# Performance work log

Hardware: AMD Instinct MI355X
Metric: run time of the kernel (lower is better)

The kernel has to match this reference:

```python
import jax, jax.numpy as jnp
import numpy as np
from jax import lax

EPS = 1e-5

def _conv(x, w, b, pad):
    y = lax.conv_general_dilated(x, w, (1, 1), [(pad, pad), (pad, pad)],
                                 dimension_numbers=('NCHW', 'OIHW', 'NCHW'))
    return y + b[None, :, None, None]

def _bn(x, g, b, m, v):
    # eval-mode BatchNorm2d with running stats
    scale = g * lax.rsqrt(v + EPS)
    return x * scale[None, :, None, None] + (b - m * scale)[None, :, None, None]

def setup_inputs() -> dict:
    key = jax.random.key(0)
    ks = jax.random.split(key, 16)
    B, C, H, W = 16, 64, 128, 128
    C2 = 2 * C
    d = {}
    d['x'] = jax.random.normal(ks[0], (B, C, H, W), jnp.float32)
    # fc1: Conv2d(C,C,3,p=1) + BN(C)
    d['fc1_w'] = jax.random.normal(ks[1], (C, C, 3, 3), jnp.float32) * 0.05
    d['fc1_b'] = jax.random.normal(ks[2], (C,), jnp.float32) * 0.05
    d['bn1_g'] = jnp.ones((C,), jnp.float32)
    d['bn1_b'] = jnp.zeros((C,), jnp.float32)
    d['bn1_m'] = jax.random.normal(ks[3], (C,), jnp.float32) * 0.05
    d['bn1_v'] = jax.random.uniform(ks[4], (C,), jnp.float32) * 0.5 + 0.5
    # graph_conv.nn: Conv2d(2C,2C,1) + BN(2C) + GELU
    d['gc_w'] = jax.random.normal(ks[5], (C2, C2, 1, 1), jnp.float32) * 0.05
    d['gc_b'] = jax.random.normal(ks[6], (C2,), jnp.float32) * 0.05
    d['bng_g'] = jnp.ones((C2,), jnp.float32)
    d['bng_b'] = jnp.zeros((C2,), jnp.float32)
    d['bng_m'] = jax.random.normal(ks[7], (C2,), jnp.float32) * 0.05
    d['bng_v'] = jax.random.uniform(ks[8], (C2,), jnp.float32) * 0.5 + 0.5
    # fc2: Conv2d(2C,C,3,p=1) + BN(C)
    d['fc2_w'] = jax.random.normal(ks[9], (C, C2, 3, 3), jnp.float32) * 0.05
    d['fc2_b'] = jax.random.normal(ks[10], (C,), jnp.float32) * 0.05
    d['bn2_g'] = jnp.ones((C,), jnp.float32)
    d['bn2_b'] = jnp.zeros((C,), jnp.float32)
    d['bn2_m'] = jax.random.normal(ks[11], (C,), jnp.float32) * 0.05
    d['bn2_v'] = jax.random.uniform(ks[12], (C,), jnp.float32) * 0.5 + 0.5
    return d

def reference(x, fc1_w, fc1_b, bn1_g, bn1_b, bn1_m, bn1_v,
              gc_w, gc_b, bng_g, bng_b, bng_m, bng_v,
              fc2_w, fc2_b, bn2_g, bn2_b, bn2_m, bn2_v):
    # fc1
    h = _bn(_conv(x, fc1_w, fc1_b, 1), bn1_g, bn1_b, bn1_m, bn1_v)
    # MRConv4dSP: strided self-attention over superpatch tokens
    sel = h[:, :, ::4, ::4]                          # [B,C,h4,w4]
    B, C, h4, w4 = sel.shape
    q = sel.reshape(B, C, h4 * w4).transpose(0, 2, 1)  # [B,N,C]
    scale = C ** (-0.5)
    att = jax.nn.softmax(jnp.einsum('bnc,bmc->bnm', q, q) * scale, axis=-1)
    o = jnp.einsum('bnm,bmc->bnc', att, q)           # [B,N,C]
    o = o.transpose(0, 2, 1).reshape(B, C, h4, w4)
    o = jnp.repeat(jnp.repeat(o, 4, axis=2), 4, axis=3)
    g = jnp.concatenate([h, o], axis=1)              # [B,2C,H,W]
    g = jax.nn.gelu(_bn(_conv(g, gc_w, gc_b, 0), bng_g, bng_b, bng_m, bng_v),
                    approximate=False)
    # fc2 + residual (drop_path=0 -> identity)
    y = _bn(_conv(g, fc2_w, fc2_b, 1), bn2_g, bn2_b, bn2_m, bn2_v)
    return y + x
```

## Files before the change

### kernel.cpp

```cpp
#include <hip/hip_runtime.h>
#include <math.h>

#define EPSV 1e-5f

typedef __bf16 bf16;
using bf16x8 = __attribute__((ext_vector_type(8))) __bf16;
using bf16x4 = __attribute__((ext_vector_type(4))) __bf16;
using bf16x2 = __attribute__((ext_vector_type(2))) __bf16;
using f32x4  = __attribute__((ext_vector_type(4))) float;

static __device__ __forceinline__ f32x4 mfma16(bf16x8 a, bf16x8 b, f32x4 c) {
    return __builtin_amdgcn_mfma_f32_16x16x32_bf16(a, b, c, 0, 0, 0);
}
static __device__ __forceinline__ f32x4 zero4() {
    f32x4 z = {0.f, 0.f, 0.f, 0.f};
    return z;
}

typedef __attribute__((address_space(1))) const char g_char_t;
typedef __attribute__((address_space(3))) char lds_char_t;
static __device__ __forceinline__ void gll16(const void* g, void* l) {
    __builtin_amdgcn_global_load_lds((g_char_t*)g, (lds_char_t*)l, 16, 0, 0);
}

static __device__ __forceinline__ float gelu_f(float v) {
    float z = fabsf(v) * 0.70710678118f;
    float t = __builtin_amdgcn_rcpf(1.f + 0.3275911f * z);
    float poly = t * (0.254829592f + t * (-0.284496736f + t * (1.421413741f +
                 t * (-1.453152027f + t * 1.061405429f))));
    float e = __expf(-z * z);
    float erfv = copysignf(1.f - poly * e, v);
    return 0.5f * v * (1.f + erfv);
}

static __device__ __forceinline__ void prep3x3_one(const float* w, bf16* wt,
                                                   int t, int CIN)
{
    int cout = t / CIN, ci = t - cout * CIN;
    int cci = ci >> 5, lg = (ci >> 3) & 3, j = ci & 7;
    int mi = cout >> 4, lix = cout & 15;
#pragma unroll
    for (int kgt = 0; kgt < 9; ++kgt) {
        float v = w[(size_t)t * 9 + kgt];
        wt[((((size_t)kgt * (CIN >> 5) + cci) * 4 + mi) * 64 + lg * 16 + lix) * 8 + j]
            = (bf16)v;
    }
}

__global__ __launch_bounds__(256) void prep_all(
    const float* __restrict__ fc1_w, const float* __restrict__ fc2_w,
    const float* __restrict__ gc_w,
    bf16* __restrict__ wt1, bf16* __restrict__ wt2, bf16* __restrict__ wtg,
    float* __restrict__ zb)
{
    int bx = blockIdx.x, tid = threadIdx.x;
    if (bx < 16) {
        prep3x3_one(fc1_w, wt1, bx * 256 + tid, 64);
    } else if (bx < 48) {
        prep3x3_one(fc2_w, wt2, (bx - 16) * 256 + tid, 128);
    } else {
        if (bx == 48 && tid < 64)
            ((float4*)zb)[tid] = make_float4(0.f, 0.f, 0.f, 0.f);
        int t = (bx - 48) * 256 + tid;
        int cout = t >> 7, ci = t & 127;
        int ks = ci >> 5, lg = (ci >> 3) & 3, j = ci & 7;
        wtg[(((size_t)(ks * 4 + lg) * 128) + cout) * 8 + j] = (bf16)gc_w[t];
    }
}

__global__ __launch_bounds__(256) void cvt_x_nhwc(const float* __restrict__ x,
                                                  bf16* __restrict__ xb)
{
    __shared__ float t_lds[64 * 68];
    const int bx = blockIdx.x;
    const int b  = blockIdx.y;
    const int y  = bx >> 1, x0 = (bx & 1) * 64;
    const int tid = threadIdx.x;

    for (int f = tid; f < 64 * 16; f += 256) {
        int c = f >> 4, xu = f & 15;
        float4 v = *(const float4*)&x[((size_t)(b * 64 + c) << 14) + (y << 7) + x0 + xu * 4];
        t_lds[(xu * 4 + 0) * 68 + c] = v.x;
        t_lds[(xu * 4 + 1) * 68 + c] = v.y;
        t_lds[(xu * 4 + 2) * 68 + c] = v.z;
        t_lds[(xu * 4 + 3) * 68 + c] = v.w;
    }
    __syncthreads();
    for (int f = tid; f < 64 * 8; f += 256) {
        int xx = f >> 3, cu = f & 7;
        const float* p = &t_lds[xx * 68 + cu * 8];
        bf16x8 v;
#pragma unroll
        for (int j = 0; j < 8; ++j) v[j] = (bf16)p[j];
        *(bf16x8*)&xb[((size_t)((b * 128 + y) * 128) + x0 + xx) * 64 + cu * 8] = v;
    }
}

template<int CIN, int OUTMODE>
__global__ __launch_bounds__(512) void conv3x3_mfma(
    const bf16* __restrict__ in, const bf16* __restrict__ wt,
    const float* __restrict__ bias,
    const float* __restrict__ bg, const float* __restrict__ bb,
    const float* __restrict__ bm, const float* __restrict__ bv,
    const bf16* __restrict__ resid, const bf16* __restrict__ zb,
    void* __restrict__ outp, bf16* __restrict__ qout)
{
    constexpr int NC = CIN >> 5;
    __shared__ bf16 in_lds[2][672 * 32];
    __shared__ bf16 w_lds[2][36 * 512];

    const int wg = blockIdx.x;
    const int v  = (wg & 7) * 64 + (wg >> 3);
    const int tile = v & 31, b = v >> 5;
    const int x0 = (tile & 1) * 64;
    const int y0 = (tile >> 1) * 8;
    const int tid  = threadIdx.x;
    const int wid  = tid >> 6;
    const int lane = tid & 63;
    const int lix  = lane & 15, lg = lane >> 4;

    int goff[6]; bool gok[6];
#pragma unroll
    for (int i = 0; i < 6; ++i) {
        int chunk = wid + 8 * i;
        int f = chunk * 64 + lane;
        int pix = f >> 2, u = f & 3;
        int sw = (pix & 3) ^ ((pix >> 2) & 3);
        int ug = u ^ sw;
        int iy = pix / 66, ix = pix - iy * 66;
        int gy = y0 + iy - 1, gx = x0 + ix - 1;
        gok[i]  = (chunk < 42) && (pix < 660) &&
                  (unsigned)gy < 128u && (unsigned)gx < 128u;
        goff[i] = ((b * 128 + gy) * 128 + gx) * CIN + ug * 8;
    }
    int rd[9];
#pragma unroll
    for (int kg = 0; kg < 3; ++kg)
#pragma unroll
        for (int t = 0; t < 3; ++t) {
            int pix0 = (wid + kg) * 66 + lix + t;
            int sw = (pix0 & 3) ^ ((pix0 >> 2) & 3);
            rd[kg * 3 + t] = pix0 * 32 + ((lg ^ sw) << 3);
        }

    f32x4 acc[4][4];
#pragma unroll
    for (int i = 0; i < 4; ++i)
#pragma unroll
        for (int j = 0; j < 4; ++j) acc[i][j] = zero4();

    auto issue_in = [&](int cci, int buf) {
#pragma unroll
        for (int i = 0; i < 6; ++i) {
            int chunk = wid + 8 * i;
            if (chunk < 42) {
                const void* src = gok[i] ? (const void*)(in + goff[i] + cci * 32)
                                         : (const void*)zb;
                gll16(src, (char*)&in_lds[buf][0] + chunk * 1024);
            }
        }
    };
    auto issue_w = [&](int cci, int buf) {
#pragma unroll
        for (int i = 0; i < 5; ++i) {
            int chunk = wid + 8 * i;
            if (chunk < 36) {
                const bf16* src = wt + ((size_t)(chunk >> 2) * NC + cci) * 2048
                                     + (chunk & 3) * 512 + lane * 8;
                gll16(src, (char*)&w_lds[buf][0] + chunk * 1024);
            }
        }
    };
    auto compute = [&](int buf) {
        bf16x8 afA[4], bfA[4], afB[4], bfB[4];
#pragma unroll
        for (int mi = 0; mi < 4; ++mi)
            afA[mi] = *(const bf16x8*)&w_lds[buf][(0 * 4 + mi) * 512 + lane * 8];
#pragma unroll
        for (int nj = 0; nj < 4; ++nj)
            bfA[nj] = *(const bf16x8*)&in_lds[buf][rd[0] + nj * 512];
#pragma unroll
        for (int kgt = 0; kgt < 9; ++kgt) {
            bf16x8* afC = (kgt & 1) ? afB : afA;
            bf16x8* bfC = (kgt & 1) ? bfB : bfA;
            bf16x8* afN = (kgt & 1) ? afA : afB;
            bf16x8* bfN = (kgt & 1) ? bfA : bfB;
            if (kgt < 8) {
#pragma unroll
                for (int mi = 0; mi < 4; ++mi)
                    afN[mi] = *(const bf16x8*)&w_lds[buf][((kgt + 1) * 4 + mi) * 512 + lane * 8];
#pragma unroll
                for (int nj = 0; nj < 4; ++nj)
                    bfN[nj] = *(const bf16x8*)&in_lds[buf][rd[kgt + 1] + nj * 512];
            }
            __builtin_amdgcn_sched_barrier(0);
#pragma unroll
            for (int nj = 0; nj < 4; ++nj)
#pragma unroll
                for (int mi = 0; mi < 4; ++mi)
                    acc[mi][nj] = mfma16(afC[mi], bfC[nj], acc[mi][nj]);
            __builtin_amdgcn_sched_barrier(0);
        }
    };

    issue_in(0, 0);
    issue_w(0, 0);
#pragma unroll 1
    for (int c = 0; c < NC; ++c) {
        if (c + 1 < NC) {
            issue_in(c + 1, (c + 1) & 1);
            issue_w(c + 1, (c + 1) & 1);
            if (wid < 2)      asm volatile("s_waitcnt vmcnt(11)" ::: "memory");
            else if (wid < 4) asm volatile("s_waitcnt vmcnt(10)" ::: "memory");
            else              asm volatile("s_waitcnt vmcnt(9)"  ::: "memory");
        } else {
            asm volatile("s_waitcnt vmcnt(0)" ::: "memory");
        }
        __builtin_amdgcn_s_barrier();
        __builtin_amdgcn_sched_barrier(0);
        compute(c & 1);
        __builtin_amdgcn_s_barrier();
    }

    if (OUTMODE == 0) {
        bf16* out = (bf16*)outp;
        bf16* stg = &in_lds[0][0];
#pragma unroll
        for (int mi = 0; mi < 4; ++mi) {
            float A[4], Bc[4];
#pragma unroll
            for (int r = 0; r < 4; ++r) {
                int c = mi * 16 + lg * 4 + r;
                float s = bg[c] * rsqrtf(bv[c] + EPSV);
                A[r]  = s;
                Bc[r] = bias[c] * s + bb[c] - bm[c] * s;
            }
#pragma unroll
            for (int nj = 0; nj < 4; ++nj) {
                int px = nj * 16 + lix;
                bf16x4 vv;
#pragma unroll
                for (int r = 0; r < 4; ++r)
                    vv[r] = (bf16)(acc[mi][nj][r] * A[r] + Bc[r]);
                *(bf16x4*)&stg[(wid * 64 + px) * 68 + mi * 16 + lg * 4] = vv;
            }
        }
        __syncthreads();
#pragma unroll
        for (int k = 0; k < 8; ++k) {
            int idx = k * 512 + tid;
            int row = idx >> 9, rem = idx & 511;
            int px = rem >> 3, cu = rem & 7;
            bf16x8 vv = *(const bf16x8*)&stg[(row * 64 + px) * 68 + cu * 8];
            *(bf16x8*)&out[((size_t)((b * 128 + y0 + row) * 128)
                            + x0 + px) * 64 + cu * 8] = vv;
        }
        if (qout && tid < 256) {
            int row4 = (tid >> 7) * 4;
            int rem  = tid & 127;
            int px4  = (rem >> 3) * 4, cu = rem & 7;
            int gy = y0 + row4, gx = x0 + px4;
            int n = ((gy >> 2) << 5) + (gx >> 2);
            bf16x8 vv = *(const bf16x8*)&stg[(row4 * 64 + px4) * 68 + cu * 8];
            *(bf16x8*)&qout[((size_t)(b * 1024 + n)) * 64 + cu * 8] = vv;
        }
    } else {
        float* out = (float*)outp;
        const int gy = y0 + wid;
#pragma unroll
        for (int mi = 0; mi < 4; ++mi) {
            float A[4], Bc[4];
#pragma unroll
            for (int r = 0; r < 4; ++r) {
                int c = mi * 16 + lg * 4 + r;
                float s = bg[c] * rsqrtf(bv[c] + EPSV);
                A[r]  = s;
                Bc[r] = bias[c] * s + bb[c] - bm[c] * s;
            }
#pragma unroll
            for (int nj = 0; nj < 4; ++nj) {
                int px = x0 + nj * 16 + lix;
                bf16x4 rv = *(const bf16x4*)&resid[((size_t)((b * 128 + gy) * 128) + px) * 64
                                                   + mi * 16 + lg * 4];
#pragma unroll
                for (int r = 0; r < 4; ++r) {
                    int c = mi * 16 + lg * 4 + r;
                    size_t oi = ((size_t)(b * 64 + c) << 14) + (gy << 7) + px;
                    out[oi] = acc[mi][nj][r] * A[r] + Bc[r] + (float)rv[r];
                }
            }
        }
    }
}

__global__ __launch_bounds__(256) void attn_fused(const bf16* __restrict__ q,
                                                  bf16* __restrict__ o)
{
    __shared__ bf16 qn[64 * 72];
    __shared__ bf16 kn[128 * 72];
    __shared__ bf16 vt[64 * 136];
    __shared__ bf16 pl[4][16 * 136];
    __shared__ __align__(16) float fac[4][16];
    const int n0 = blockIdx.x * 64, b = blockIdx.y;
    const int tid = threadIdx.x, w = tid >> 6, lane = tid & 63;
    const int lix = lane & 15, lg = lane >> 4;
    const bf16* qb = q + ((size_t)b << 16);

    for (int f = tid; f < 512; f += 256) {
        int row = f >> 3, cu = f & 7;
        *(bf16x8*)&qn[row * 72 + cu * 8] =
            *(const bf16x8*)&qb[(size_t)(n0 + row) * 64 + cu * 8];
    }

    float m_run = -3.0e38f, l_run = 0.f;
    f32x4 oacc[4];
#pragma unroll
    for (int ct = 0; ct < 4; ++ct) oacc[ct] = zero4();

    for (int mt = 0; mt < 1024; mt += 128) {
        __syncthreads();
        for (int f = tid; f < 1024; f += 256) {
            int row = f >> 3, cu = f & 7;
            *(bf16x8*)&kn[row * 72 + cu * 8] =
                *(const bf16x8*)&qb[(size_t)(mt + row) * 64 + cu * 8];
        }
        for (int f = tid; f < 512; f += 256) {
            int mp = f >> 3, cu = f & 7;
            int m = mp * 2;
            bf16x8 a = *(const bf16x8*)&qb[(size_t)(mt + m) * 64 + cu * 8];
            bf16x8 c = *(const bf16x8*)&qb[(size_t)(mt + m + 1) * 64 + cu * 8];
#pragma unroll
            for (int j = 0; j < 8; ++j) {
                bf16x2 pr = {a[j], c[j]};
                *(bf16x2*)&vt[(cu * 8 + j) * 136 + m] = pr;
            }
        }
        __syncthreads();

        bf16x8 bq0 = *(const bf16x8*)&qn[(w * 16 + lix) * 72 + lg * 8];
        bf16x8 bq1 = *(const bf16x8*)&qn[(w * 16 + lix) * 72 + 32 + lg * 8];

        f32x4 s[8];
#pragma unroll
        for (int t = 0; t < 8; ++t) {
            bf16x8 a0 = *(const bf16x8*)&kn[(t * 16 + lix) * 72 + lg * 8];
            bf16x8 a1 = *(const bf16x8*)&kn[(t * 16 + lix) * 72 + 32 + lg * 8];
            s[t] = mfma16(a0, bq0, zero4());
            s[t] = mfma16(a1, bq1, s[t]);
        }

        float mx = -3.0e38f;
#pragma unroll
        for (int t = 0; t < 8; ++t)
#pragma unroll
            for (int r = 0; r < 4; ++r) { s[t][r] *= 0.125f; mx = fmaxf(mx, s[t][r]); }
        mx = fmaxf(mx, __shfl_xor(mx, 16));
        mx = fmaxf(mx, __shfl_xor(mx, 32));
        float m_new = fmaxf(m_run, mx);
        float alpha = __expf(m_run - m_new);

        float psum = 0.f;
#pragma unroll
        for (int t = 0; t < 8; ++t) {
            float p0 = __expf(s[t][0] - m_new), p1 = __expf(s[t][1] - m_new);
            float p2 = __expf(s[t][2] - m_new), p3 = __expf(s[t][3] - m_new);
            psum += (p0 + p1) + (p2 + p3);
            bf16x2 v01 = {(bf16)p0, (bf16)p1};
            bf16x2 v23 = {(bf16)p2, (bf16)p3};
            *(bf16x2*)&pl[w][lix * 136 + t * 16 + lg * 4]     = v01;
            *(bf16x2*)&pl[w][lix * 136 + t * 16 + lg * 4 + 2] = v23;
        }
        psum += __shfl_xor(psum, 16);
        psum += __shfl_xor(psum, 32);
        l_run = l_run * alpha + psum;
        m_run = m_new;
        if (lg == 0) fac[w][lix] = alpha;

        float4 a4 = *(const float4*)&fac[w][lg * 4];
        float aa[4] = {a4.x, a4.y, a4.z, a4.w};
#pragma unroll
        for (int ct = 0; ct < 4; ++ct)
#pragma unroll
            for (int r = 0; r < 4; ++r) oacc[ct][r] *= aa[r];

#pragma unroll
        for (int kk = 0; kk < 4; ++kk) {
            bf16x8 pa = *(const bf16x8*)&pl[w][lix * 136 + kk * 32 + lg * 8];
#pragma unroll
            for (int ct = 0; ct < 4; ++ct) {
                bf16x8 bv = *(const bf16x8*)&vt[(ct * 16 + lix) * 136 + kk * 32 + lg * 8];
                oacc[ct] = mfma16(pa, bv, oacc[ct]);
            }
        }
    }

    if (lg == 0) fac[w][lix] = l_run;
    float4 l4 = *(const float4*)&fac[w][lg * 4];
    float ll[4] = {1.f / l4.x, 1.f / l4.y, 1.f / l4.z, 1.f / l4.w};
#pragma unroll
    for (int ct = 0; ct < 4; ++ct)
#pragma unroll
        for (int r = 0; r < 4; ++r) {
            int n = n0 + w * 16 + lg * 4 + r;
            int c = ct * 16 + lix;
            o[((size_t)(b * 1024 + n)) * 64 + c] = (bf16)(oacc[ct][r] * ll[r]);
        }
}

__global__ __launch_bounds__(256) void conv1x1_mfma(
    const bf16* __restrict__ h, const bf16* __restrict__ ov,
    const bf16* __restrict__ wt, const float* __restrict__ bias,
    const float* __restrict__ bg, const float* __restrict__ bb,
    const float* __restrict__ bm, const float* __restrict__ bv,
    bf16* __restrict__ g)
{
    __shared__ bf16 in1[128 * 136];
    const int y = blockIdx.x, b = blockIdx.y;
    const int tid = threadIdx.x;
    const int wid = tid >> 6, lane = tid & 63;
    const int lix = lane & 15, lg = lane >> 4;
    const int wm = wid >> 1, wn = wid & 1;

    for (int f = tid; f < 128 * 16; f += 256) {
        int px = f >> 4, cu = f & 15;
        bf16x8 v;
        if (cu < 8) {
            v = *(const bf16x8*)&h[((size_t)((b * 128 + y) * 128 + px)) * 64 + cu * 8];
        } else {
            int n = ((y >> 2) << 5) + (px >> 2);
            v = *(const bf16x8*)&ov[((size_t)(b * 1024 + n)) * 64 + (cu - 8) * 8];
        }
        *(bf16x8*)&in1[px * 136 + cu * 8] = v;
    }
    __syncthreads();

    f32x4 acc[4][4];
#pragma unroll
    for (int i = 0; i < 4; ++i)
#pragma unroll
        for (int j = 0; j < 4; ++j) acc[i][j] = zero4();

#pragma unroll
    for (int ks = 0; ks < 4; ++ks) {
        bf16x8 af[4], bfv[4];
#pragma unroll
        for (int mi = 0; mi < 4; ++mi)
            af[mi] = *(const bf16x8*)&wt[(((size_t)(ks * 4 + lg) * 128) + wm * 64 + mi * 16 + lix) * 8];
#pragma unroll
        for (int nj = 0; nj < 4; ++nj)
            bfv[nj] = *(const bf16x8*)&in1[(wn * 64 + nj * 16 + lix) * 136 + ks * 32 + lg * 8];
#pragma unroll
        for (int mi = 0; mi < 4; ++mi)
#pragma unroll
            for (int nj = 0; nj < 4; ++nj)
                acc[mi][nj] = mfma16(af[mi], bfv[nj], acc[mi][nj]);
    }

    __syncthreads();
    bf16* stg = in1;
#pragma unroll
    for (int mi = 0; mi < 4; ++mi) {
        float A[4], Bc[4];
#pragma unroll
        for (int r = 0; r < 4; ++r) {
            int c = wm * 64 + mi * 16 + lg * 4 + r;
            float s = bg[c] * rsqrtf(bv[c] + EPSV);
            A[r]  = s;
            Bc[r] = bias[c] * s + bb[c] - bm[c] * s;
        }
#pragma unroll
        for (int nj = 0; nj < 4; ++nj) {
            int px = wn * 64 + nj * 16 + lix;
            bf16x4 vv;
#pragma unroll
            for (int r = 0; r < 4; ++r)
                vv[r] = (bf16)gelu_f(acc[mi][nj][r] * A[r] + Bc[r]);
            *(bf16x4*)&stg[px * 132 + wm * 64 + mi * 16 + lg * 4] = vv;
        }
    }
    __syncthreads();
#pragma unroll
    for (int k = 0; k < 8; ++k) {
        int idx = k * 256 + tid;
        int px = idx >> 4, cu = idx & 15;
        bf16x8 v = *(const bf16x8*)&stg[px * 132 + cu * 8];
        *(bf16x8*)&g[((size_t)((b * 128 + y) * 128) + px) * 128 + cu * 8] = v;
    }
}

extern "C" void kernel_launch(void* const* d_in, const int* in_sizes, int n_in,
                              void* d_out, int out_size, void* d_ws, size_t ws_size,
                              hipStream_t stream)
{
    const float* x     = (const float*)d_in[0];
    const float* fc1_w = (const float*)d_in[1];
    const float* fc1_b = (const float*)d_in[2];
    const float* bn1_g = (const float*)d_in[3];
    const float* bn1_b = (const float*)d_in[4];
    const float* bn1_m = (const float*)d_in[5];
    const float* bn1_v = (const float*)d_in[6];
    const float* gc_w  = (const float*)d_in[7];
    const float* gc_b  = (const float*)d_in[8];
    const float* bng_g = (const float*)d_in[9];
    const float* bng_b = (const float*)d_in[10];
    const float* bng_m = (const float*)d_in[11];
    const float* bng_v = (const float*)d_in[12];
    const float* fc2_w = (const float*)d_in[13];
    const float* fc2_b = (const float*)d_in[14];
    const float* bn2_g = (const float*)d_in[15];
    const float* bn2_b = (const float*)d_in[16];
    const float* bn2_m = (const float*)d_in[17];
    const float* bn2_v = (const float*)d_in[18];

    char* wsb = (char*)d_ws;
    bf16* x_bf = (bf16*)wsb;
    bf16* h    = (bf16*)(wsb + 33554432);
    bf16* g    = (bf16*)(wsb + 67108864);
    bf16* q    = (bf16*)(wsb + 134217728);
    bf16* o    = (bf16*)(wsb + 136314880);
    bf16* wt1  = (bf16*)(wsb + 138412032);
    bf16* wt2  = (bf16*)(wsb + 138485760);
    bf16* wtg  = (bf16*)(wsb + 138633216);
    bf16* zb   = (bf16*)(wsb + 138665984);

    prep_all<<<112, 256, 0, stream>>>(fc1_w, fc2_w, gc_w, wt1, wt2, wtg,
                                      (float*)zb);

    cvt_x_nhwc<<<dim3(256, 16), 256, 0, stream>>>(x, x_bf);

    conv3x3_mfma<64, 0><<<512, 512, 0, stream>>>(
        x_bf, wt1, fc1_b, bn1_g, bn1_b, bn1_m, bn1_v, nullptr, zb, h, q);

    attn_fused<<<dim3(16, 16), 256, 0, stream>>>(q, o);

    conv1x1_mfma<<<dim3(128, 16), 256, 0, stream>>>(
        h, o, wtg, gc_b, bng_g, bng_b, bng_m, bng_v, g);

    conv3x3_mfma<128, 1><<<512, 512, 0, stream>>>(
        g, wt2, fc2_b, bn2_g, bn2_b, bn2_m, bn2_v, x_bf, zb, (float*)d_out, nullptr);
}
```

Before: 179.4 us.

## Fuse 1x1 conv+BN+GELU into attention kernel and merge prep with input conversion

The attention kernel now keeps its output tile in LDS and computes the 1x1 graph conv, BN and GELU for the 8 rows of pixels that correspond to its 64 tokens. It streams h through a double-buffered global_load_lds pipeline with swizzled layout. This removes the o round-trip through global memory and one launch. The weight-prep and x conversion kernels are also merged into a single launch. The trade-off is that the fused 1x1 conv now runs on only 256 blocks instead of 2048, which reduces parallelism for that stage.

```diff
diff --git a/kernel.cpp b/kernel.cpp
--- a/kernel.cpp
+++ b/kernel.cpp
@@ -47,52 +47,49 @@
     }
 }
 
-__global__ __launch_bounds__(256) void prep_all(
+__global__ __launch_bounds__(256) void prep_cvt(
+    const float* __restrict__ x, bf16* __restrict__ xb,
     const float* __restrict__ fc1_w, const float* __restrict__ fc2_w,
     const float* __restrict__ gc_w,
     bf16* __restrict__ wt1, bf16* __restrict__ wt2, bf16* __restrict__ wtg,
     float* __restrict__ zb)
 {
-    int bx = blockIdx.x, tid = threadIdx.x;
-    if (bx < 16) {
-        prep3x3_one(fc1_w, wt1, bx * 256 + tid, 64);
-    } else if (bx < 48) {
-        prep3x3_one(fc2_w, wt2, (bx - 16) * 256 + tid, 128);
+    __shared__ float t_lds[64 * 68];
+    const int bx = blockIdx.x, tid = threadIdx.x;
+    if (bx < 4096) {
+        const int b = bx >> 8, inner = bx & 255;
+        const int y = inner >> 1, x0 = (inner & 1) * 64;
+        for (int f = tid; f < 64 * 16; f += 256) {
+            int c = f >> 4, xu = f & 15;
+            float4 v = *(const float4*)&x[((size_t)(b * 64 + c) << 14) + (y << 7) + x0 + xu * 4];
+            t_lds[(xu * 4 + 0) * 68 + c] = v.x;
+            t_lds[(xu * 4 + 1) * 68 + c] = v.y;
+            t_lds[(xu * 4 + 2) * 68 + c] = v.z;
+            t_lds[(xu * 4 + 3) * 68 + c] = v.w;
+        }
+        __syncthreads();
+        for (int f = tid; f < 64 * 8; f += 256) {
+            int xx = f >> 3, cu = f & 7;
+            const float* p = &t_lds[xx * 68 + cu * 8];
+            bf16x8 v;
+#pragma unroll
+            for (int j = 0; j < 8; ++j) v[j] = (bf16)p[j];
+            *(bf16x8*)&xb[((size_t)((b * 128 + y) * 128) + x0 + xx) * 64 + cu * 8] = v;
+        }
     } else {
-        if (bx == 48 && tid < 64)
-            ((float4*)zb)[tid] = make_float4(0.f, 0.f, 0.f, 0.f);
-        int t = (bx - 48) * 256 + tid;
-        int cout = t >> 7, ci = t & 127;
-        int ks = ci >> 5, lg = (ci >> 3) & 3, j = ci & 7;
-        wtg[(((size_t)(ks * 4 + lg) * 128) + cout) * 8 + j] = (bf16)gc_w[t];
-    }
-}
-
-__global__ __launch_bounds__(256) void cvt_x_nhwc(const float* __restrict__ x,
-                                                  bf16* __restrict__ xb)
-{
-    __shared__ float t_lds[64 * 68];
-    const int bx = blockIdx.x;
-    const int b  = blockIdx.y;
-    const int y  = bx >> 1, x0 = (bx & 1) * 64;
-    const int tid = threadIdx.x;
-
-    for (int f = tid; f < 64 * 16; f += 256) {
-        int c = f >> 4, xu = f & 15;
-        float4 v = *(const float4*)&x[((size_t)(b * 64 + c) << 14) + (y << 7) + x0 + xu * 4];
-        t_lds[(xu * 4 + 0) * 68 + c] = v.x;
-        t_lds[(xu * 4 + 1) * 68 + c] = v.y;
-        t_lds[(xu * 4 + 2) * 68 + c] = v.z;
-        t_lds[(xu * 4 + 3) * 68 + c] = v.w;
-    }
-    __syncthreads();
-    for (int f = tid; f < 64 * 8; f += 256) {
-        int xx = f >> 3, cu = f & 7;
-        const float* p = &t_lds[xx * 68 + cu * 8];
-        bf16x8 v;
-#pragma unroll
-        for (int j = 0; j < 8; ++j) v[j] = (bf16)p[j];
-        *(bf16x8*)&xb[((size_t)((b * 128 + y) * 128) + x0 + xx) * 64 + cu * 8] = v;
+        int px = bx - 4096;
+        if (px < 16) {
+            prep3x3_one(fc1_w, wt1, px * 256 + tid, 64);
+        } else if (px < 48) {
+            prep3x3_one(fc2_w, wt2, (px - 16) * 256 + tid, 128);
+        } else {
+            if (px == 48 && tid < 64)
+                ((float4*)zb)[tid] = make_float4(0.f, 0.f, 0.f, 0.f);
+            int t = (px - 48) * 256 + tid;
+            int cout = t >> 7, ci = t & 127;
+            int ks = ci >> 5, lg = (ci >> 3) & 3, j = ci & 7;
+            wtg[(((size_t)(ks * 4 + lg) * 128) + cout) * 8 + j] = (bf16)gc_w[t];
+        }
     }
 }
 
@@ -293,14 +290,23 @@
     }
 }
 
-__global__ __launch_bounds__(256) void attn_fused(const bf16* __restrict__ q,
-                                                  bf16* __restrict__ o)
+__global__ __launch_bounds__(256) void attn_fused(
+    const bf16* __restrict__ q, const bf16* __restrict__ h,
+    const bf16* __restrict__ wtg, const float* __restrict__ bias,
+    const float* __restrict__ bg, const float* __restrict__ bb,
+    const float* __restrict__ bm, const float* __restrict__ bv,
+    bf16* __restrict__ g)
 {
-    __shared__ bf16 qn[64 * 72];
-    __shared__ bf16 kn[128 * 72];
-    __shared__ bf16 vt[64 * 136];
-    __shared__ bf16 pl[4][16 * 136];
-    __shared__ __align__(16) float fac[4][16];
+    __shared__ __align__(16) char smem[62976];
+    bf16* qn = (bf16*)smem;
+    bf16* kn = (bf16*)(smem + 9216);
+    bf16* vt = (bf16*)(smem + 27648);
+    bf16* pl = (bf16*)(smem + 45056);
+    float* fac = (float*)(smem + 62464);
+    bf16* o_lds = (bf16*)smem;
+    bf16* h_lds = (bf16*)(smem + 9216);
+    bf16* g_lds = (bf16*)(smem + 25600);
+
     const int n0 = blockIdx.x * 64, b = blockIdx.y;
     const int tid = threadIdx.x, w = tid >> 6, lane = tid & 63;
     const int lix = lane & 15, lg = lane >> 4;
@@ -367,16 +373,16 @@
             psum += (p0 + p1) + (p2 + p3);
             bf16x2 v01 = {(bf16)p0, (bf16)p1};
             bf16x2 v23 = {(bf16)p2, (bf16)p3};
-            *(bf16x2*)&pl[w][lix * 136 + t * 16 + lg * 4]     = v01;
-            *(bf16x2*)&pl[w][lix * 136 + t * 16 + lg * 4 + 2] = v23;
+            *(bf16x2*)&pl[w * 2176 + lix * 136 + t * 16 + lg * 4]     = v01;
+            *(bf16x2*)&pl[w * 2176 + lix * 136 + t * 16 + lg * 4 + 2] = v23;
         }
         psum += __shfl_xor(psum, 16);
         psum += __shfl_xor(psum, 32);
         l_run = l_run * alpha + psum;
         m_run = m_new;
-        if (lg == 0) fac[w][lix] = alpha;
-
-        float4 a4 = *(const float4*)&fac[w][lg * 4];
+        if (lg == 0) fac[w * 16 + lix] = alpha;
+
+        float4 a4 = *(const float4*)&fac[w * 16 + lg * 4];
         float aa[4] = {a4.x, a4.y, a4.z, a4.w};
 #pragma unroll
         for (int ct = 0; ct < 4; ++ct)
@@ -385,7 +391,7 @@
 
 #pragma unroll
         for (int kk = 0; kk < 4; ++kk) {
-            bf16x8 pa = *(const bf16x8*)&pl[w][lix * 136 + kk * 32 + lg * 8];
+            bf16x8 pa = *(const bf16x8*)&pl[w * 2176 + lix * 136 + kk * 32 + lg * 8];
 #pragma unroll
             for (int ct = 0; ct < 4; ++ct) {
                 bf16x8 bv = *(const bf16x8*)&vt[(ct * 16 + lix) * 136 + kk * 32 + lg * 8];
@@ -394,97 +400,113 @@
         }
     }
 
-    if (lg == 0) fac[w][lix] = l_run;
-    float4 l4 = *(const float4*)&fac[w][lg * 4];
+    if (lg == 0) fac[w * 16 + lix] = l_run;
+    float4 l4 = *(const float4*)&fac[w * 16 + lg * 4];
     float ll[4] = {1.f / l4.x, 1.f / l4.y, 1.f / l4.z, 1.f / l4.w};
+
+    __syncthreads();
 #pragma unroll
     for (int ct = 0; ct < 4; ++ct)
 #pragma unroll
         for (int r = 0; r < 4; ++r) {
-            int n = n0 + w * 16 + lg * 4 + r;
-            int c = ct * 16 + lix;
-            o[((size_t)(b * 1024 + n)) * 64 + c] = (bf16)(oacc[ct][r] * ll[r]);
-        }
-}
-
-__global__ __launch_bounds__(256) void conv1x1_mfma(
-    const bf16* __restrict__ h, const bf16* __restrict__ ov,
-    const bf16* __restrict__ wt, const float* __restrict__ bias,
-    const float* __restrict__ bg, const float* __restrict__ bb,
-    const float* __restrict__ bm, const float* __restrict__ bv,
-    bf16* __restrict__ g)
-{
-    __shared__ bf16 in1[128 * 136];
-    const int y = blockIdx.x, b = blockIdx.y;
-    const int tid = threadIdx.x;
-    const int wid = tid >> 6, lane = tid & 63;
-    const int lix = lane & 15, lg = lane >> 4;
-    const int wm = wid >> 1, wn = wid & 1;
-
-    for (int f = tid; f < 128 * 16; f += 256) {
-        int px = f >> 4, cu = f & 15;
-        bf16x8 v;
-        if (cu < 8) {
-            v = *(const bf16x8*)&h[((size_t)((b * 128 + y) * 128 + px)) * 64 + cu * 8];
+            int nl = w * 16 + lg * 4 + r;
+            o_lds[nl * 72 + ct * 16 + lix] = (bf16)(oacc[ct][r] * ll[r]);
+        }
+    __syncthreads();
+
+    const int ybase = n0 >> 3;
+    const int sxor = (lix >> 2) & 3;
+
+    float A2[2][4], B2[2][4];
+#pragma unroll
+    for (int mi = 0; mi < 2; ++mi)
+#pragma unroll
+        for (int r = 0; r < 4; ++r) {
+            int c = w * 32 + mi * 16 + lg * 4 + r;
+            float s = bg[c] * rsqrtf(bv[c] + EPSV);
+            A2[mi][r] = s;
+            B2[mi][r] = bias[c] * s + bb[c] - bm[c] * s;
+        }
+
+    auto issue_h = [&](int pg, int buf) {
+        int y = ybase + (pg >> 1), xg = (pg & 1) * 64;
+#pragma unroll
+        for (int i = 0; i < 2; ++i) {
+            int ch = w * 2 + i;
+            int px = ch * 8 + (lane >> 3);
+            int cu = lane & 7;
+            int cus = cu ^ ((px >> 2) & 3);
+            const bf16* src = &h[((size_t)((b * 128 + y) * 128) + xg + px) * 64 + cus * 8];
+            gll16(src, (char*)h_lds + buf * 8192 + ch * 1024);
+        }
+    };
+
+    issue_h(0, 0);
+#pragma unroll 1
+    for (int pg = 0; pg < 16; ++pg) {
+        if (pg < 15) {
+            issue_h(pg + 1, (pg + 1) & 1);
+            asm volatile("s_waitcnt vmcnt(2)" ::: "memory");
         } else {
-            int n = ((y >> 2) << 5) + (px >> 2);
-            v = *(const bf16x8*)&ov[((size_t)(b * 1024 + n)) * 64 + (cu - 8) * 8];
-        }
-        *(bf16x8*)&in1[px * 136 + cu * 8] = v;
-    }
-    __syncthreads();
-
-    f32x4 acc[4][4];
-#pragma unroll
-    for (int i = 0; i < 4; ++i)
-#pragma unroll
-        for (int j = 0; j < 4; ++j) acc[i][j] = zero4();
-
-#pragma unroll
-    for (int ks = 0; ks < 4; ++ks) {
-        bf16x8 af[4], bfv[4];
-#pragma unroll
-        for (int mi = 0; mi < 4; ++mi)
-            af[mi] = *(const bf16x8*)&wt[(((size_t)(ks * 4 + lg) * 128) + wm * 64 + mi * 16 + lix) * 8];
-#pragma unroll
-        for (int nj = 0; nj < 4; ++nj)
-            bfv[nj] = *(const bf16x8*)&in1[(wn * 64 + nj * 16 + lix) * 136 + ks * 32 + lg * 8];
-#pragma unroll
-        for (int mi = 0; mi < 4; ++mi)
-#pragma unroll
-            for (int nj = 0; nj < 4; ++nj)
-                acc[mi][nj] = mfma16(af[mi], bfv[nj], acc[mi][nj]);
-    }
-
-    __syncthreads();
-    bf16* stg = in1;
-#pragma unroll
-    for (int mi = 0; mi < 4; ++mi) {
-        float A[4], Bc[4];
-#pragma unroll
-        for (int r = 0; r < 4; ++r) {
-            int c = wm * 64 + mi * 16 + lg * 4 + r;
-            float s = bg[c] * rsqrtf(bv[c] + EPSV);
-            A[r]  = s;
-            Bc[r] = bias[c] * s + bb[c] - bm[c] * s;
-        }
-#pragma unroll
-        for (int nj = 0; nj < 4; ++nj) {
-            int px = wn * 64 + nj * 16 + lix;
-            bf16x4 vv;
-#pragma unroll
-            for (int r = 0; r < 4; ++r)
-                vv[r] = (bf16)gelu_f(acc[mi][nj][r] * A[r] + Bc[r]);
-            *(bf16x4*)&stg[px * 132 + wm * 64 + mi * 16 + lg * 4] = vv;
-        }
-    }
-    __syncthreads();
-#pragma unroll
-    for (int k = 0; k < 8; ++k) {
-        int idx = k * 256 + tid;
-        int px = idx >> 4, cu = idx & 15;
-        bf16x8 v = *(const bf16x8*)&stg[px * 132 + cu * 8];
-        *(bf16x8*)&g[((size_t)((b * 128 + y) * 128) + px) * 128 + cu * 8] = v;
+            asm volatile("s_waitcnt vmcnt(0)" ::: "memory");
+        }
+        __builtin_amdgcn_s_barrier();
+
+        const int buf = pg & 1;
+        const int nlb = (pg >> 3) * 32 + (pg & 1) * 16 + (lix >> 2);
+
+        f32x4 a2[2][4];
+#pragma unroll
+        for (int mi = 0; mi < 2; ++mi)
+#pragma unroll
+            for (int nj = 0; nj < 4; ++nj) a2[mi][nj] = zero4();
+
+#pragma unroll
+        for (int ks = 0; ks < 4; ++ks) {
+            bf16x8 af0 = *(const bf16x8*)&wtg[(((size_t)(ks * 4 + lg) * 128)
+                                               + w * 32 + lix) * 8];
+            bf16x8 af1 = *(const bf16x8*)&wtg[(((size_t)(ks * 4 + lg) * 128)
+                                               + w * 32 + 16 + lix) * 8];
+#pragma unroll
+            for (int nj = 0; nj < 4; ++nj) {
+                bf16x8 bfv;
+                if (ks < 2) {
+                    int px = nj * 16 + lix;
+                    bfv = *(const bf16x8*)&h_lds[buf * 4096 + px * 64
+                                                 + ((ks * 4 + (lg ^ sxor)) << 3)];
+                } else {
+                    int nl = nlb + nj * 4;
+                    bfv = *(const bf16x8*)&o_lds[nl * 72 + (((ks - 2) * 4 + lg) << 3)];
+                }
+                a2[0][nj] = mfma16(af0, bfv, a2[0][nj]);
+                a2[1][nj] = mfma16(af1, bfv, a2[1][nj]);
+            }
+        }
+
+#pragma unroll
+        for (int mi = 0; mi < 2; ++mi)
+#pragma unroll
+            for (int nj = 0; nj < 4; ++nj) {
+                int px = nj * 16 + lix;
+                bf16x4 vv;
+#pragma unroll
+                for (int r = 0; r < 4; ++r)
+                    vv[r] = (bf16)gelu_f(a2[mi][nj][r] * A2[mi][r] + B2[mi][r]);
+                *(bf16x4*)&g_lds[px * 132 + w * 32 + mi * 16 + lg * 4] = vv;
+            }
+        __builtin_amdgcn_s_barrier();
+
+        {
+            int y = ybase + (pg >> 1), xg = (pg & 1) * 64;
+#pragma unroll
+            for (int k = 0; k < 4; ++k) {
+                int idx = k * 256 + tid;
+                int px = idx >> 4, cu = idx & 15;
+                bf16x8 vv = *(const bf16x8*)&g_lds[px * 132 + cu * 8];
+                *(bf16x8*)&g[((size_t)((b * 128 + y) * 128) + xg + px) * 128 + cu * 8] = vv;
+            }
+        }
+        __builtin_amdgcn_s_barrier();
     }
 }
 
@@ -517,24 +539,19 @@
     bf16* h    = (bf16*)(wsb + 33554432);
     bf16* g    = (bf16*)(wsb + 67108864);
     bf16* q    = (bf16*)(wsb + 134217728);
-    bf16* o    = (bf16*)(wsb + 136314880);
-    bf16* wt1  = (bf16*)(wsb + 138412032);
-    bf16* wt2  = (bf16*)(wsb + 138485760);
-    bf16* wtg  = (bf16*)(wsb + 138633216);
-    bf16* zb   = (bf16*)(wsb + 138665984);
-
-    prep_all<<<112, 256, 0, stream>>>(fc1_w, fc2_w, gc_w, wt1, wt2, wtg,
-                                      (float*)zb);
-
-    cvt_x_nhwc<<<dim3(256, 16), 256, 0, stream>>>(x, x_bf);
+    bf16* wt1  = (bf16*)(wsb + 136314880);
+    bf16* wt2  = (bf16*)(wsb + 136388608);
+    bf16* wtg  = (bf16*)(wsb + 136536064);
+    bf16* zb   = (bf16*)(wsb + 136568832);
+
+    prep_cvt<<<4208, 256, 0, stream>>>(x, x_bf, fc1_w, fc2_w, gc_w,
+                                       wt1, wt2, wtg, (float*)zb);
 
     conv3x3_mfma<64, 0><<<512, 512, 0, stream>>>(
         x_bf, wt1, fc1_b, bn1_g, bn1_b, bn1_m, bn1_v, nullptr, zb, h, q);
 
-    attn_fused<<<dim3(16, 16), 256, 0, stream>>>(q, o);
-
-    conv1x1_mfma<<<dim3(128, 16), 256, 0, stream>>>(
-        h, o, wtg, gc_b, bng_g, bng_b, bng_m, bng_v, g);
+    attn_fused<<<dim3(16, 16), 256, 0, stream>>>(
+        q, h, wtg, gc_b, bng_g, bng_b, bng_m, bng_v, g);
 
     conv3x3_mfma<128, 1><<<512, 512, 0, stream>>>(
         g, wt2, fc2_b, bn2_g, bn2_b, bn2_m, bn2_v, x_bf, zb, (float*)d_out, nullptr);
```

Result: faster. 173.5 us (-3.3%).
